# Kernel tuning notes

Hardware: AMD Instinct MI355X
Metric: run time of the kernel (lower is better)

## Reference

```python
import jax, jax.numpy as jnp
import numpy as np

T, Z, D_DIM = 8, 2048, 1024
N_EXP, P_SLOT, H = 64, 32, 1024
LN_EPS = 1e-5


def setup_inputs() -> dict:
    key = jax.random.key(0)
    k = jax.random.split(key, 5)
    s = 0.02
    return {
        "x": jax.random.normal(k[0], (T, Z, D_DIM), dtype=jnp.float32),
        "phi_w": jax.random.normal(k[1], (N_EXP * P_SLOT, D_DIM), dtype=jnp.float32) * s,
        "phi_b": jax.random.normal(k[2], (N_EXP * P_SLOT,), dtype=jnp.float32) * s,
        "expert_w": jax.random.normal(k[3], (N_EXP, D_DIM, H), dtype=jnp.float32) * s,
        "expert_b": jax.random.normal(k[4], (N_EXP, H), dtype=jnp.float32) * s,
    }


def reference(x, phi_w, phi_b, expert_w, expert_b):
    t, z, d = x.shape
    n = expert_w.shape[0]
    p = phi_w.shape[0] // n
    # routing logits: [t, z, n, p]
    logits = (jnp.einsum('tzd,ed->tze', x, phi_w) + phi_b).reshape(t, z, n, p)
    D = jax.nn.softmax(logits, axis=3)  # dispatch: softmax over slots p
    C = jax.nn.softmax(logits, axis=2)  # combine:  softmax over experts n
    # slot inputs, summed over batch AND tokens (as in the source einsum)
    X_tilde = jnp.einsum('tznp,tzd->npd', D, x)
    X_tilde = jnp.clip(X_tilde, -33000.0, 65000.0)
    # layer norm over last dim, no affine
    mu = jnp.mean(X_tilde, axis=-1, keepdims=True)
    var = jnp.mean(jnp.square(X_tilde - mu), axis=-1, keepdims=True)
    X_tilde = (X_tilde - mu) * jax.lax.rsqrt(var + LN_EPS)
    X_tilde = jnp.tanh(X_tilde)
    # per-expert Linear, batched over experts: [n,p,d] x [n,d,H] -> [n,p,H]
    Y_tilde = jnp.einsum('npd,ndH->npH', X_tilde, expert_w) + expert_b[:, None, :]
    # combine back to tokens: [t,z,H]
    Y = jnp.einsum('tznp,npH->tzH', C, Y_tilde)
    return Y
```

## Files before the change

kernel.cpp:

```cpp
#include <hip/hip_runtime.h>
#include <hip/hip_bf16.h>
#include <math.h>

#define TOKENS   16384
#define DDIM     1024
#define NEXP     64
#define PSLOT    32
#define NSLOTS   2048
#define HDIM     1024
#define LN_EPS   1e-5f
#define KSPLIT   8

typedef __bf16 b16x8 __attribute__((ext_vector_type(8)));
typedef float  f32x4 __attribute__((ext_vector_type(4)));

__device__ __forceinline__ unsigned short f2b(float f) {
    union { float f; unsigned u; } v; v.f = f;
    unsigned r = v.u + 0x7FFF + ((v.u >> 16) & 1);
    return (unsigned short)(r >> 16);
}

__device__ __forceinline__ void load_lds16(const void* g, void* l) {
    __builtin_amdgcn_global_load_lds(
        (const __attribute__((address_space(1))) void*)g,
        (__attribute__((address_space(3))) void*)l, 16, 0, 0);
}

template<bool BIAS>
__global__ __launch_bounds__(512, 2) void gemm_nt_256(
    const unsigned short* __restrict__ A,
    const unsigned short* __restrict__ B,
    const float* __restrict__ bias,
    float* __restrict__ C,
    int M, int N, int K)
{
    __shared__ unsigned short lds[2][2][256 * 64];
    const int tid  = threadIdx.x;
    const int wave = tid >> 6;
    const int lane = tid & 63;
    const int wr = wave >> 2;
    const int wc = wave & 3;
    const int fr = lane & 15;
    const int fs = lane >> 4;
    const int kswz = ((lane & 7) ^ (lane >> 3)) * 8;
    const int m0 = blockIdx.y * 256;
    const int n0 = blockIdx.x * 256;

    const int kc = K / gridDim.z;
    const int kb = blockIdx.z * kc;
    C += (size_t)blockIdx.z * M * N;
    const int NT = kc >> 6;

    f32x4 acc[8][4] = {};
    b16x8 Ag[4][2], Bf[2][2], Bs2[2][2];

#define KOF(T)   (kb + ((T) < NT ? (T) : (NT - 1)) * 64)

#define STAGE_A(BUF, T, R0) { \
    const int k0_ = KOF(T); \
    _Pragma("unroll") for (int hh = 0; hh < 2; ++hh) { \
        const int rp_ = (R0) + hh * 64 + wave * 8 + (lane >> 3); \
        const int L_  = ((rp_ >> 6) & 1) * 128 + ((rp_ >> 7) & 1) * 64 + (rp_ & 63); \
        load_lds16(A + (size_t)(m0 + L_) * K + k0_ + kswz, \
                   &lds[BUF][0][((R0) + hh * 64 + wave * 8) * 64]); } }

#define STAGE_B(BUF, T, R0) { \
    const int k0_ = KOF(T); \
    _Pragma("unroll") for (int hh = 0; hh < 2; ++hh) { \
        const int rp_ = (R0) + hh * 64 + wave * 8 + (lane >> 3); \
        const int L_  = ((rp_ >> 5) & 3) * 64 + ((rp_ >> 7) & 1) * 32 + (rp_ & 31); \
        load_lds16(B + (size_t)(n0 + L_) * K + k0_ + kswz, \
                   &lds[BUF][1][((R0) + hh * 64 + wave * 8) * 64]); } }

#define LDA_G(BUF, IBASE) \
    _Pragma("unroll") for (int ii = 0; ii < 4; ++ii) { \
        const int rp_ = (IBASE) + 64 * wr + ii * 16 + fr; \
        _Pragma("unroll") for (int h = 0; h < 2; ++h) \
            Ag[ii][h] = *(const b16x8*)&lds[BUF][0][rp_ * 64 + (((h * 4 + fs) ^ (rp_ & 7)) * 8)]; }

#define LDB_G(BUF, JBASE, DST) \
    _Pragma("unroll") for (int jj = 0; jj < 2; ++jj) { \
        const int rp_ = (JBASE) + 32 * wc + jj * 16 + fr; \
        _Pragma("unroll") for (int h = 0; h < 2; ++h) \
            DST[jj][h] = *(const b16x8*)&lds[BUF][1][rp_ * 64 + (((h * 4 + fs) ^ (rp_ & 7)) * 8)]; }

#define MFMA_Q(IB, JB, BREG) \
    __builtin_amdgcn_s_setprio(1); \
    _Pragma("unroll") for (int ii = 0; ii < 4; ++ii) \
    _Pragma("unroll") for (int jj = 0; jj < 2; ++jj) \
    _Pragma("unroll") for (int h = 0; h < 2; ++h) \
        acc[(IB) + ii][(JB) + jj] = __builtin_amdgcn_mfma_f32_16x16x32_bf16( \
            Ag[ii][h], BREG[jj][h], acc[(IB) + ii][(JB) + jj], 0, 0, 0); \
    __builtin_amdgcn_s_setprio(0);

#define BAR1  { __builtin_amdgcn_s_barrier(); __builtin_amdgcn_sched_barrier(0); }
#define BAR2  { __builtin_amdgcn_s_barrier(); }
#define VMW6  { asm volatile("s_waitcnt vmcnt(6)" ::: "memory"); \
                __builtin_amdgcn_sched_barrier(0); }

    STAGE_A(0, 0, 0);   STAGE_B(0, 0, 0);   STAGE_B(0, 0, 128);  STAGE_A(0, 0, 128);
    STAGE_A(1, 1, 0);   STAGE_B(1, 1, 0);   STAGE_B(1, 1, 128);
    VMW6; BAR2;

    const int nit = NT >> 1;
    for (int it = 0; it < nit; ++it) {
        const int t1 = 2 * it + 1;
        LDA_G(0, 0); LDB_G(0, 0, Bf);
        STAGE_A(1, t1, 128);
        BAR1; MFMA_Q(0, 0, Bf); BAR2;
        LDB_G(0, 128, Bs2);
        STAGE_A(0, t1 + 1, 0);
        BAR1; MFMA_Q(0, 2, Bs2); BAR2;
        LDA_G(0, 128);
        STAGE_B(0, t1 + 1, 0);
        BAR1; MFMA_Q(4, 2, Bs2); BAR2;
        STAGE_B(0, t1 + 1, 128);
        BAR1; MFMA_Q(4, 0, Bf); VMW6; BAR2;
        LDA_G(1, 0); LDB_G(1, 0, Bf);
        STAGE_A(0, t1 + 1, 128);
        BAR1; MFMA_Q(0, 0, Bf); BAR2;
        LDB_G(1, 128, Bs2);
        STAGE_A(1, t1 + 2, 0);
        BAR1; MFMA_Q(0, 2, Bs2); BAR2;
        LDA_G(1, 128);
        STAGE_B(1, t1 + 2, 0);
        BAR1; MFMA_Q(4, 2, Bs2); BAR2;
        STAGE_B(1, t1 + 2, 128);
        BAR1; MFMA_Q(4, 0, Bf); VMW6; BAR2;
    }

    const int col  = lane & 15;
    const int row4 = (lane >> 4) * 4;
#pragma unroll
    for (int j = 0; j < 4; ++j) {
        const int n = n0 + wc * 64 + j * 16 + col;
        const float bj = BIAS ? bias[n] : 0.f;
#pragma unroll
        for (int i = 0; i < 8; ++i) {
#pragma unroll
            for (int r = 0; r < 4; ++r) {
                const int m = m0 + wr * 128 + i * 16 + row4 + r;
                C[(size_t)m * N + n] = acc[i][j][r] + bj;
            }
        }
    }
#undef KOF
#undef STAGE_A
#undef STAGE_B
#undef LDA_G
#undef LDB_G
#undef MFMA_Q
#undef BAR1
#undef BAR2
#undef VMW6
}

__global__ __launch_bounds__(256) void prep_x(
    const float* __restrict__ in, unsigned short* __restrict__ xb,
    unsigned short* __restrict__ xT)
{
    __shared__ unsigned short tile[64][68];
    const int t  = threadIdx.x;
    const int c0 = blockIdx.x * 64;
    const int r0 = blockIdx.y * 64;
    const int tr = t >> 4, tc4 = (t & 15) * 4;
#pragma unroll
    for (int i = 0; i < 4; ++i) {
        const int r = tr + i * 16;
        const float4 v = *(const float4*)&in[(size_t)(r0 + r) * DDIM + c0 + tc4];
        ushort4 o;
        o.x = f2b(v.x); o.y = f2b(v.y); o.z = f2b(v.z); o.w = f2b(v.w);
        *(ushort4*)&xb[(size_t)(r0 + r) * DDIM + c0 + tc4] = o;
        tile[tc4 + 0][r] = o.x; tile[tc4 + 1][r] = o.y;
        tile[tc4 + 2][r] = o.z; tile[tc4 + 3][r] = o.w;
    }
    __syncthreads();
#pragma unroll
    for (int i = 0; i < 4; ++i) {
        const int r = tr + i * 16;
        ushort4 o;
        o.x = tile[r][tc4 + 0]; o.y = tile[r][tc4 + 1];
        o.z = tile[r][tc4 + 2]; o.w = tile[r][tc4 + 3];
        *(ushort4*)&xT[(size_t)(c0 + r) * TOKENS + r0 + tc4] = o;
    }
}

__global__ __launch_bounds__(256) void cast_f32_bf16(
    const float* __restrict__ in, unsigned short* __restrict__ out)
{
    const size_t i = (size_t)(blockIdx.x * 256 + threadIdx.x) * 8;
    const float4 a = *(const float4*)&in[i];
    const float4 b = *(const float4*)&in[i + 4];
    ushort4 o0, o1;
    o0.x = f2b(a.x); o0.y = f2b(a.y); o0.z = f2b(a.z); o0.w = f2b(a.w);
    o1.x = f2b(b.x); o1.y = f2b(b.y); o1.z = f2b(b.z); o1.w = f2b(b.w);
    *(ushort4*)&out[i]     = o0;
    *(ushort4*)&out[i + 4] = o1;
}

template<typename TIN>
__global__ __launch_bounds__(256) void transpose_cast(
    const TIN* __restrict__ in, unsigned short* __restrict__ out, int R, int C)
{
    __shared__ unsigned short tile[64][68];
    const int t  = threadIdx.x;
    const int r0 = blockIdx.y * 64, c0 = blockIdx.x * 64;
    const int tr = t >> 4, tc4 = (t & 15) * 4;
#pragma unroll
    for (int i = 0; i < 4; ++i) {
        const int r = tr + i * 16;
        const TIN* p = in + (size_t)(r0 + r) * C + c0 + tc4;
        if constexpr (sizeof(TIN) == 4) {
            const float4 v = *(const float4*)p;
            tile[tc4 + 0][r] = f2b(v.x); tile[tc4 + 1][r] = f2b(v.y);
            tile[tc4 + 2][r] = f2b(v.z); tile[tc4 + 3][r] = f2b(v.w);
        } else {
            const ushort4 v = *(const ushort4*)p;
            tile[tc4 + 0][r] = v.x; tile[tc4 + 1][r] = v.y;
            tile[tc4 + 2][r] = v.z; tile[tc4 + 3][r] = v.w;
        }
    }
    __syncthreads();
#pragma unroll
    for (int i = 0; i < 4; ++i) {
        const int r = tr + i * 16;
        ushort4 o;
        o.x = tile[r][tc4 + 0]; o.y = tile[r][tc4 + 1];
        o.z = tile[r][tc4 + 2]; o.w = tile[r][tc4 + 3];
        *(ushort4*)&out[(size_t)(c0 + r) * R + r0 + tc4] = o;
    }
}

__global__ __launch_bounds__(256) void softmax_dc(
    const float* __restrict__ logits,
    unsigned short* __restrict__ Db, unsigned short* __restrict__ Cb)
{
    __shared__ float ls[NEXP * 33];
    __shared__ float dmax[NEXP], dinv[NEXP];
    __shared__ float cmax[PSLOT], cinv[PSLOT];
    const int tid = threadIdx.x;
    const size_t base = (size_t)blockIdx.x * NSLOTS;

#pragma unroll
    for (int i = 0; i < 8; ++i) {
        const int e = tid + i * 256;
        ls[e + (e >> 5)] = logits[base + e];
    }
    __syncthreads();

    if (tid < 64) {
        const float* r = &ls[tid * 33];
        float m = r[0];
#pragma unroll
        for (int p = 1; p < PSLOT; ++p) m = fmaxf(m, r[p]);
        float s = 0.f;
#pragma unroll
        for (int p = 0; p < PSLOT; ++p) s += __expf(r[p] - m);
        dmax[tid] = m; dinv[tid] = 1.f / s;
    } else if (tid < 96) {
        const int p = tid - 64;
        float m = ls[p];
#pragma unroll
        for (int n = 1; n < NEXP; ++n) m = fmaxf(m, ls[n * 33 + p]);
        float s = 0.f;
#pragma unroll
        for (int n = 0; n < NEXP; ++n) s += __expf(ls[n * 33 + p] - m);
        cmax[p] = m; cinv[p] = 1.f / s;
    }
    __syncthreads();

#pragma unroll
    for (int i = 0; i < 8; ++i) {
        const int e = tid + i * 256;
        const int n = e >> 5, p = e & 31;
        const float l = ls[e + n];
        Db[base + e] = f2b(__expf(l - dmax[n]) * dinv[n]);
        Cb[base + e] = f2b(__expf(l - cmax[p]) * cinv[p]);
    }
}

__global__ __launch_bounds__(256) void reduce_ln_tanh(
    const float* __restrict__ parts, float* __restrict__ Xt)
{
    const int tid = threadIdx.x;
    const size_t off = (size_t)blockIdx.x * DDIM + tid * 4;
    __shared__ float red1[4], red2[4];

    float4 v = *(const float4*)&parts[off];
#pragma unroll
    for (int s = 1; s < KSPLIT; ++s) {
        const float4 p = *(const float4*)&parts[(size_t)s * NSLOTS * DDIM + off];
        v.x += p.x; v.y += p.y; v.z += p.z; v.w += p.w;
    }
    v.x = fminf(fmaxf(v.x, -33000.f), 65000.f);
    v.y = fminf(fmaxf(v.y, -33000.f), 65000.f);
    v.z = fminf(fmaxf(v.z, -33000.f), 65000.f);
    v.w = fminf(fmaxf(v.w, -33000.f), 65000.f);

    float s = v.x + v.y + v.z + v.w;
#pragma unroll
    for (int off2 = 32; off2 > 0; off2 >>= 1) s += __shfl_down(s, off2);
    if ((tid & 63) == 0) red1[tid >> 6] = s;
    __syncthreads();
    const float mu = (red1[0] + red1[1] + red1[2] + red1[3]) * (1.f / DDIM);

    const float dx = v.x - mu, dy = v.y - mu, dz = v.z - mu, dw = v.w - mu;
    float q = dx * dx + dy * dy + dz * dz + dw * dw;
#pragma unroll
    for (int off2 = 32; off2 > 0; off2 >>= 1) q += __shfl_down(q, off2);
    if ((tid & 63) == 0) red2[tid >> 6] = q;
    __syncthreads();
    const float var = (red2[0] + red2[1] + red2[2] + red2[3]) * (1.f / DDIM);
    const float sc = rsqrtf(var + LN_EPS);

    float4 o;
    o.x = tanhf(dx * sc); o.y = tanhf(dy * sc);
    o.z = tanhf(dz * sc); o.w = tanhf(dw * sc);
    *(float4*)&Xt[off] = o;
}

__global__ __launch_bounds__(256) void expert_gemm(
    const float* __restrict__ Xt, const float* __restrict__ W,
    const float* __restrict__ bias, float* __restrict__ Yt)
{
    const int n   = blockIdx.y;
    const int h0  = blockIdx.x * 64;
    const int tid = threadIdx.x;
    __shared__ float As[32][17];
    __shared__ float Bs[16][68];

    const int r  = tid >> 3;
    const int c8 = (tid & 7) * 8;
    float acc[8];
#pragma unroll
    for (int j = 0; j < 8; ++j) acc[j] = 0.f;

    const float* Wn = W + (size_t)n * DDIM * HDIM;
    for (int k0 = 0; k0 < DDIM; k0 += 16) {
        if (tid < 128) {
            const int row = tid >> 2, c4 = (tid & 3) * 4;
            const float4 v = *(const float4*)&Xt[(size_t)(n * 32 + row) * DDIM + k0 + c4];
            As[row][c4 + 0] = v.x; As[row][c4 + 1] = v.y;
            As[row][c4 + 2] = v.z; As[row][c4 + 3] = v.w;
        }
        {
            const int row = tid >> 4, c4 = (tid & 15) * 4;
            *(float4*)&Bs[row][c4] =
                *(const float4*)&Wn[(size_t)(k0 + row) * HDIM + h0 + c4];
        }
        __syncthreads();
#pragma unroll
        for (int kk = 0; kk < 16; ++kk) {
            const float a = As[r][kk];
            const float4 b0 = *(const float4*)&Bs[kk][c8];
            const float4 b1 = *(const float4*)&Bs[kk][c8 + 4];
            acc[0] = fmaf(a, b0.x, acc[0]); acc[1] = fmaf(a, b0.y, acc[1]);
            acc[2] = fmaf(a, b0.z, acc[2]); acc[3] = fmaf(a, b0.w, acc[3]);
            acc[4] = fmaf(a, b1.x, acc[4]); acc[5] = fmaf(a, b1.y, acc[5]);
            acc[6] = fmaf(a, b1.z, acc[6]); acc[7] = fmaf(a, b1.w, acc[7]);
        }
        __syncthreads();
    }

    float4 o0, o1;
    const float* bn = bias + (size_t)n * HDIM + h0 + c8;
    o0.x = acc[0] + bn[0]; o0.y = acc[1] + bn[1];
    o0.z = acc[2] + bn[2]; o0.w = acc[3] + bn[3];
    o1.x = acc[4] + bn[4]; o1.y = acc[5] + bn[5];
    o1.z = acc[6] + bn[6]; o1.w = acc[7] + bn[7];
    float* outp = Yt + (size_t)(n * 32 + r) * HDIM + h0 + c8;
    *(float4*)&outp[0] = o0;
    *(float4*)&outp[4] = o1;
}

extern "C" void kernel_launch(void* const* d_in, const int* in_sizes, int n_in,
                              void* d_out, int out_size, void* d_ws, size_t ws_size,
                              hipStream_t stream)
{
    const float* x        = (const float*)d_in[0];
    const float* phi_w    = (const float*)d_in[1];
    const float* phi_b    = (const float*)d_in[2];
    const float* expert_w = (const float*)d_in[3];
    const float* expert_b = (const float*)d_in[4];
    float* out = (float*)d_out;

    char* ws = (char*)d_ws;
    const size_t MB = 1u << 20;
    unsigned short* xb     = (unsigned short*)(ws);
    unsigned short* xT     = (unsigned short*)(ws +  32 * MB);
    unsigned short* pwb    = (unsigned short*)(ws +  64 * MB);
    float*          logits = (float*)(ws +  68 * MB);
    unsigned short* Db     = (unsigned short*)(ws + 196 * MB);
    unsigned short* Cb     = (unsigned short*)(ws + 260 * MB);
    unsigned short* DbT    = (unsigned short*)(ws + 324 * MB);
    float*          parts  = (float*)(ws + 388 * MB);
    float*          Xt     = (float*)(ws + 452 * MB);
    float*          Yt     = (float*)(ws + 460 * MB);
    unsigned short* YtT    = (unsigned short*)(ws + 468 * MB);

    prep_x<<<dim3(DDIM / 64, TOKENS / 64), 256, 0, stream>>>(x, xb, xT);
    cast_f32_bf16<<<NSLOTS * DDIM / (256 * 8), 256, 0, stream>>>(phi_w, pwb);

    gemm_nt_256<true><<<dim3(NSLOTS / 256, TOKENS / 256), 512, 0, stream>>>(
        xb, pwb, phi_b, logits, TOKENS, NSLOTS, DDIM);

    softmax_dc<<<TOKENS, 256, 0, stream>>>(logits, Db, Cb);

    transpose_cast<unsigned short><<<dim3(NSLOTS / 64, TOKENS / 64), 256, 0, stream>>>(
        Db, DbT, TOKENS, NSLOTS);

    gemm_nt_256<false>
        <<<dim3(DDIM / 256, NSLOTS / 256, KSPLIT), 512, 0, stream>>>(
            DbT, xT, nullptr, parts, NSLOTS, DDIM, TOKENS);

    reduce_ln_tanh<<<NSLOTS, 256, 0, stream>>>(parts, Xt);

    expert_gemm<<<dim3(HDIM / 64, NEXP), 256, 0, stream>>>(
        Xt, expert_w, expert_b, Yt);

    transpose_cast<float><<<dim3(HDIM / 64, NSLOTS / 64), 256, 0, stream>>>(
        Yt, YtT, NSLOTS, HDIM);

    gemm_nt_256<false><<<dim3(HDIM / 256, TOKENS / 256), 512, 0, stream>>>(
        Cb, YtT, nullptr, out, TOKENS, HDIM, NSLOTS);
}
```

Baseline: 773.2 us.

## Fuse transposes into softmax and expert kernels, swizzle GEMM tiles, peel last iteration

The dispatch softmax now writes its output already transposed, and the expert GEMM writes a transposed bf16 result. This removes two separate transpose_cast launches and their round trips through global memory. The combine softmax is split into its own kernel and spreads the per-slot reductions over all 256 threads. The 256x256 GEMM gains a workgroup-index swizzle for L2 locality and a peeled final iteration, which removes redundant clamped prefetches. In exchange, logits are read twice by two kernels, and the dispatch kernel writes with a strided pattern.

```diff
diff --git a/kernel.cpp b/kernel.cpp
--- a/kernel.cpp
+++ b/kernel.cpp
@@ -43,8 +43,13 @@
     const int fr = lane & 15;
     const int fs = lane >> 4;
     const int kswz = ((lane & 7) ^ (lane >> 3)) * 8;
-    const int m0 = blockIdx.y * 256;
-    const int n0 = blockIdx.x * 256;
+
+    const int gx  = (int)gridDim.x, gy = (int)gridDim.y;
+    const int nwg = gx * gy;
+    const int wg  = (int)blockIdx.y * gx + (int)blockIdx.x;
+    const int swz = (wg & 7) * (nwg >> 3) + (wg >> 3);
+    const int m0 = (swz / gx) * 256;
+    const int n0 = (swz % gx) * 256;
 
     const int kc = K / gridDim.z;
     const int kb = blockIdx.z * kc;
@@ -54,7 +59,7 @@
     f32x4 acc[8][4] = {};
     b16x8 Ag[4][2], Bf[2][2], Bs2[2][2];
 
-#define KOF(T)   (kb + ((T) < NT ? (T) : (NT - 1)) * 64)
+#define KOF(T)   (kb + (T) * 64)
 
 #define STAGE_A(BUF, T, R0) { \
     const int k0_ = KOF(T); \
@@ -97,13 +102,15 @@
 #define BAR2  { __builtin_amdgcn_s_barrier(); }
 #define VMW6  { asm volatile("s_waitcnt vmcnt(6)" ::: "memory"); \
                 __builtin_amdgcn_sched_barrier(0); }
+#define VMW0  { asm volatile("s_waitcnt vmcnt(0)" ::: "memory"); \
+                __builtin_amdgcn_sched_barrier(0); }
 
     STAGE_A(0, 0, 0);   STAGE_B(0, 0, 0);   STAGE_B(0, 0, 128);  STAGE_A(0, 0, 128);
     STAGE_A(1, 1, 0);   STAGE_B(1, 1, 0);   STAGE_B(1, 1, 128);
     VMW6; BAR2;
 
     const int nit = NT >> 1;
-    for (int it = 0; it < nit; ++it) {
+    for (int it = 0; it < nit - 1; ++it) {
         const int t1 = 2 * it + 1;
         LDA_G(0, 0); LDB_G(0, 0, Bf);
         STAGE_A(1, t1, 128);
@@ -129,6 +136,25 @@
         BAR1; MFMA_Q(4, 0, Bf); VMW6; BAR2;
     }
 
+    {
+        const int t1 = NT - 1;
+        LDA_G(0, 0); LDB_G(0, 0, Bf);
+        STAGE_A(1, t1, 128);
+        BAR1; MFMA_Q(0, 0, Bf); BAR2;
+        LDB_G(0, 128, Bs2);
+        BAR1; MFMA_Q(0, 2, Bs2); BAR2;
+        LDA_G(0, 128);
+        BAR1; MFMA_Q(4, 2, Bs2); BAR2;
+        BAR1; MFMA_Q(4, 0, Bf); VMW0; BAR2;
+        LDA_G(1, 0); LDB_G(1, 0, Bf);
+        BAR1; MFMA_Q(0, 0, Bf); BAR2;
+        LDB_G(1, 128, Bs2);
+        BAR1; MFMA_Q(0, 2, Bs2); BAR2;
+        LDA_G(1, 128);
+        BAR1; MFMA_Q(4, 2, Bs2); BAR2;
+        BAR1; MFMA_Q(4, 0, Bf); BAR2;
+    }
+
     const int col  = lane & 15;
     const int row4 = (lane >> 4) * 4;
 #pragma unroll
@@ -153,6 +179,7 @@
 #undef BAR1
 #undef BAR2
 #undef VMW6
+#undef VMW0
 }
 
 __global__ __launch_bounds__(256) void prep_x(
@@ -198,46 +225,45 @@
     *(ushort4*)&out[i + 4] = o1;
 }
 
-template<typename TIN>
-__global__ __launch_bounds__(256) void transpose_cast(
-    const TIN* __restrict__ in, unsigned short* __restrict__ out, int R, int C)
-{
-    __shared__ unsigned short tile[64][68];
-    const int t  = threadIdx.x;
-    const int r0 = blockIdx.y * 64, c0 = blockIdx.x * 64;
-    const int tr = t >> 4, tc4 = (t & 15) * 4;
-#pragma unroll
-    for (int i = 0; i < 4; ++i) {
-        const int r = tr + i * 16;
-        const TIN* p = in + (size_t)(r0 + r) * C + c0 + tc4;
-        if constexpr (sizeof(TIN) == 4) {
-            const float4 v = *(const float4*)p;
-            tile[tc4 + 0][r] = f2b(v.x); tile[tc4 + 1][r] = f2b(v.y);
-            tile[tc4 + 2][r] = f2b(v.z); tile[tc4 + 3][r] = f2b(v.w);
-        } else {
-            const ushort4 v = *(const ushort4*)p;
-            tile[tc4 + 0][r] = v.x; tile[tc4 + 1][r] = v.y;
-            tile[tc4 + 2][r] = v.z; tile[tc4 + 3][r] = v.w;
-        }
-    }
-    __syncthreads();
-#pragma unroll
-    for (int i = 0; i < 4; ++i) {
-        const int r = tr + i * 16;
-        ushort4 o;
-        o.x = tile[r][tc4 + 0]; o.y = tile[r][tc4 + 1];
-        o.z = tile[r][tc4 + 2]; o.w = tile[r][tc4 + 3];
-        *(ushort4*)&out[(size_t)(c0 + r) * R + r0 + tc4] = o;
-    }
-}
-
-__global__ __launch_bounds__(256) void softmax_dc(
-    const float* __restrict__ logits,
-    unsigned short* __restrict__ Db, unsigned short* __restrict__ Cb)
+__global__ __launch_bounds__(256) void dispatch_T(
+    const float* __restrict__ logits, unsigned short* __restrict__ DbT)
+{
+    __shared__ float ls[8 * 1057];
+    const int tid  = threadIdx.x;
+    const int tok0 = blockIdx.x * 32;
+    const int s0   = blockIdx.y * 256;
+
+#pragma unroll
+    for (int i = 0; i < 8; ++i) {
+        const int flat = i * 256 + tid;
+        const int row  = flat >> 6;
+        const int c4   = (flat & 63) * 4;
+        const float4 v = *(const float4*)&logits[(size_t)(tok0 + row) * NSLOTS + s0 + c4];
+        float* b = &ls[(c4 >> 5) * 1057 + row * 33 + (c4 & 31)];
+        b[0] = v.x; b[1] = v.y; b[2] = v.z; b[3] = v.w;
+    }
+    __syncthreads();
+
+    const int tok = tid & 31, n = tid >> 5;
+    const float* r = &ls[n * 1057 + tok * 33];
+    float m = r[0];
+#pragma unroll
+    for (int p = 1; p < PSLOT; ++p) m = fmaxf(m, r[p]);
+    float s = 0.f;
+#pragma unroll
+    for (int p = 0; p < PSLOT; ++p) s += __expf(r[p] - m);
+    const float inv = 1.f / s;
+    unsigned short* o = &DbT[(size_t)(s0 + n * 32) * TOKENS + tok0 + tok];
+#pragma unroll
+    for (int p = 0; p < PSLOT; ++p)
+        o[(size_t)p * TOKENS] = f2b(__expf(r[p] - m) * inv);
+}
+
+__global__ __launch_bounds__(256) void combine_softmax(
+    const float* __restrict__ logits, unsigned short* __restrict__ Cb)
 {
     __shared__ float ls[NEXP * 33];
-    __shared__ float dmax[NEXP], dinv[NEXP];
-    __shared__ float cmax[PSLOT], cinv[PSLOT];
+    __shared__ float pm[8][32], ps[8][32];
     const int tid = threadIdx.x;
     const size_t base = (size_t)blockIdx.x * NSLOTS;
 
@@ -248,34 +274,28 @@
     }
     __syncthreads();
 
-    if (tid < 64) {
-        const float* r = &ls[tid * 33];
-        float m = r[0];
-#pragma unroll
-        for (int p = 1; p < PSLOT; ++p) m = fmaxf(m, r[p]);
-        float s = 0.f;
-#pragma unroll
-        for (int p = 0; p < PSLOT; ++p) s += __expf(r[p] - m);
-        dmax[tid] = m; dinv[tid] = 1.f / s;
-    } else if (tid < 96) {
-        const int p = tid - 64;
-        float m = ls[p];
-#pragma unroll
-        for (int n = 1; n < NEXP; ++n) m = fmaxf(m, ls[n * 33 + p]);
-        float s = 0.f;
-#pragma unroll
-        for (int n = 0; n < NEXP; ++n) s += __expf(ls[n * 33 + p] - m);
-        cmax[p] = m; cinv[p] = 1.f / s;
-    }
-    __syncthreads();
-
-#pragma unroll
-    for (int i = 0; i < 8; ++i) {
-        const int e = tid + i * 256;
-        const int n = e >> 5, p = e & 31;
-        const float l = ls[e + n];
-        Db[base + e] = f2b(__expf(l - dmax[n]) * dinv[n]);
-        Cb[base + e] = f2b(__expf(l - cmax[p]) * cinv[p]);
+    const int p = tid & 31, sub = tid >> 5;
+    float m = ls[(sub * 8) * 33 + p];
+#pragma unroll
+    for (int k = 1; k < 8; ++k) m = fmaxf(m, ls[(sub * 8 + k) * 33 + p]);
+    float s = 0.f;
+#pragma unroll
+    for (int k = 0; k < 8; ++k) s += __expf(ls[(sub * 8 + k) * 33 + p] - m);
+    pm[sub][p] = m; ps[sub][p] = s;
+    __syncthreads();
+
+    float M = pm[0][p];
+#pragma unroll
+    for (int k = 1; k < 8; ++k) M = fmaxf(M, pm[k][p]);
+    float S = 0.f;
+#pragma unroll
+    for (int k = 0; k < 8; ++k) S += ps[k][p] * __expf(pm[k][p] - M);
+    const float cinv = 1.f / S;
+
+#pragma unroll
+    for (int k = 0; k < 8; ++k) {
+        const int n = sub * 8 + k;
+        Cb[base + n * 32 + p] = f2b(__expf(ls[n * 33 + p] - M) * cinv);
     }
 }
 
@@ -321,13 +341,14 @@
 
 __global__ __launch_bounds__(256) void expert_gemm(
     const float* __restrict__ Xt, const float* __restrict__ W,
-    const float* __restrict__ bias, float* __restrict__ Yt)
+    const float* __restrict__ bias, unsigned short* __restrict__ YtT)
 {
     const int n   = blockIdx.y;
     const int h0  = blockIdx.x * 64;
     const int tid = threadIdx.x;
     __shared__ float As[32][17];
     __shared__ float Bs[16][68];
+    __shared__ unsigned short ty[64][36];
 
     const int r  = tid >> 3;
     const int c8 = (tid & 7) * 8;
@@ -362,15 +383,18 @@
         __syncthreads();
     }
 
-    float4 o0, o1;
-    const float* bn = bias + (size_t)n * HDIM + h0 + c8;
-    o0.x = acc[0] + bn[0]; o0.y = acc[1] + bn[1];
-    o0.z = acc[2] + bn[2]; o0.w = acc[3] + bn[3];
-    o1.x = acc[4] + bn[4]; o1.y = acc[5] + bn[5];
-    o1.z = acc[6] + bn[6]; o1.w = acc[7] + bn[7];
-    float* outp = Yt + (size_t)(n * 32 + r) * HDIM + h0 + c8;
-    *(float4*)&outp[0] = o0;
-    *(float4*)&outp[4] = o1;
+    const float* bn = bias + (size_t)n * HDIM + h0;
+#pragma unroll
+    for (int j = 0; j < 8; ++j)
+        ty[c8 + j][r] = f2b(acc[j] + bn[c8 + j]);
+    __syncthreads();
+
+    const int row = tid >> 2, q = (tid & 3) * 8;
+    const ushort4 u0 = *(const ushort4*)&ty[row][q];
+    const ushort4 u1 = *(const ushort4*)&ty[row][q + 4];
+    unsigned short* dst = &YtT[(size_t)(h0 + row) * NSLOTS + n * 32 + q];
+    *(ushort4*)&dst[0] = u0;
+    *(ushort4*)&dst[4] = u1;
 }
 
 extern "C" void kernel_launch(void* const* d_in, const int* in_sizes, int n_in,
@@ -390,13 +414,11 @@
     unsigned short* xT     = (unsigned short*)(ws +  32 * MB);
     unsigned short* pwb    = (unsigned short*)(ws +  64 * MB);
     float*          logits = (float*)(ws +  68 * MB);
-    unsigned short* Db     = (unsigned short*)(ws + 196 * MB);
+    unsigned short* DbT    = (unsigned short*)(ws + 196 * MB);
     unsigned short* Cb     = (unsigned short*)(ws + 260 * MB);
-    unsigned short* DbT    = (unsigned short*)(ws + 324 * MB);
-    float*          parts  = (float*)(ws + 388 * MB);
-    float*          Xt     = (float*)(ws + 452 * MB);
-    float*          Yt     = (float*)(ws + 460 * MB);
-    unsigned short* YtT    = (unsigned short*)(ws + 468 * MB);
+    float*          parts  = (float*)(ws + 324 * MB);
+    float*          Xt     = (float*)(ws + 388 * MB);
+    unsigned short* YtT    = (unsigned short*)(ws + 396 * MB);
 
     prep_x<<<dim3(DDIM / 64, TOKENS / 64), 256, 0, stream>>>(x, xb, xT);
     cast_f32_bf16<<<NSLOTS * DDIM / (256 * 8), 256, 0, stream>>>(phi_w, pwb);
@@ -404,10 +426,9 @@
     gemm_nt_256<true><<<dim3(NSLOTS / 256, TOKENS / 256), 512, 0, stream>>>(
         xb, pwb, phi_b, logits, TOKENS, NSLOTS, DDIM);
 
-    softmax_dc<<<TOKENS, 256, 0, stream>>>(logits, Db, Cb);
-
-    transpose_cast<unsigned short><<<dim3(NSLOTS / 64, TOKENS / 64), 256, 0, stream>>>(
-        Db, DbT, TOKENS, NSLOTS);
+    dispatch_T<<<dim3(TOKENS / 32, NSLOTS / 256), 256, 0, stream>>>(logits, DbT);
+
+    combine_softmax<<<TOKENS, 256, 0, stream>>>(logits, Cb);
 
     gemm_nt_256<false>
         <<<dim3(DDIM / 256, NSLOTS / 256, KSPLIT), 512, 0, stream>>>(
@@ -416,10 +437,7 @@
     reduce_ln_tanh<<<NSLOTS, 256, 0, stream>>>(parts, Xt);
 
     expert_gemm<<<dim3(HDIM / 64, NEXP), 256, 0, stream>>>(
-        Xt, expert_w, expert_b, Yt);
-
-    transpose_cast<float><<<dim3(HDIM / 64, NSLOTS / 64), 256, 0, stream>>>(
-        Yt, YtT, NSLOTS, HDIM);
+        Xt, expert_w, expert_b, YtT);
 
     gemm_nt_256<false><<<dim3(HDIM / 256, TOKENS / 256), 512, 0, stream>>>(
         Cb, YtT, nullptr, out, TOKENS, HDIM, NSLOTS);
```

Result: no change. 780.6 us (+1.0%).
